# Kernel optimization log

Hardware: AMD Instinct MI355X
Metric: run time of the kernel (lower is better)

The kernel has to match this reference:

```python
import jax, jax.numpy as jnp
import numpy as np

DIM = 32          # d_model == channel dim of the volume
D_STATE = 16
D_CONV = 4
EXPAND = 2
D_INNER = EXPAND * DIM        # 64
DT_RANK = max(1, (DIM + 15) // 16)  # ceil(d_model/16) = 2
LN_EPS = 1e-5


def setup_inputs() -> dict:
    key = jax.random.key(0)
    ks = jax.random.split(key, 12)
    B, Dd, Hh, Ww = 1, 32, 32, 32
    sc = 0.02
    x = jax.random.normal(ks[0], (B, DIM, Dd, Hh, Ww), jnp.float32)
    ln_w = jnp.ones((DIM,), jnp.float32)
    ln_b = jnp.zeros((DIM,), jnp.float32)
    in_proj_w = jax.random.normal(ks[1], (2 * D_INNER, DIM), jnp.float32) * sc
    conv_w = jax.random.normal(ks[2], (D_INNER, 1, D_CONV), jnp.float32) * sc
    conv_b = jnp.zeros((D_INNER,), jnp.float32)
    x_proj_w = jax.random.normal(ks[3], (DT_RANK + 2 * D_STATE, D_INNER), jnp.float32) * sc
    dt_proj_w = jax.random.normal(ks[4], (D_INNER, DT_RANK), jnp.float32) * sc
    dt_proj_b = jax.random.uniform(ks[5], (D_INNER,), jnp.float32, -4.0, -2.0)  # small softplus(dt) at init
    # Mamba S4D-real init: A = -[1..d_state], stored as A_log
    A_log = jnp.log(jnp.broadcast_to(jnp.arange(1, D_STATE + 1, dtype=jnp.float32), (D_INNER, D_STATE)))
    D_param = jnp.ones((D_INNER,), jnp.float32)
    out_proj_w = jax.random.normal(ks[6], (DIM, D_INNER), jnp.float32) * sc
    return {
        "x": x, "ln_w": ln_w, "ln_b": ln_b, "in_proj_w": in_proj_w,
        "conv_w": conv_w, "conv_b": conv_b, "x_proj_w": x_proj_w,
        "dt_proj_w": dt_proj_w, "dt_proj_b": dt_proj_b, "A_log": A_log,
        "D_param": D_param, "out_proj_w": out_proj_w,
    }


def _mamba_layer(x, ln_w, ln_b, in_proj_w, conv_w, conv_b, x_proj_w,
                 dt_proj_w, dt_proj_b, A_log, D_param, out_proj_w):
    B, C, Dd, Hh, Ww = x.shape
    L = Dd * Hh * Ww
    # z-scan flatten: (B, C, D, H, W) -> (B, L, C)
    xf = x.reshape(B, C, L).transpose(0, 2, 1)
    # LayerNorm over channel dim
    mu = jnp.mean(xf, axis=-1, keepdims=True)
    var = jnp.mean(jnp.square(xf - mu), axis=-1, keepdims=True)
    xn = (xf - mu) * jax.lax.rsqrt(var + LN_EPS) * ln_w + ln_b
    # in_proj -> x, z branches
    xz = xn @ in_proj_w.T                      # (B, L, 2*d_inner)
    x_in, z = jnp.split(xz, 2, axis=-1)
    # depthwise causal conv1d over sequence
    xt = x_in.transpose(0, 2, 1)               # (B, d_inner, L)
    xc = jax.lax.conv_general_dilated(
        xt, conv_w, window_strides=(1,), padding=[(D_CONV - 1, 0)],
        feature_group_count=D_INNER)
    xc = jax.nn.silu(xc + conv_b[None, :, None]).transpose(0, 2, 1)  # (B, L, d_inner)
    # input-dependent dt, B, C
    x_dbl = xc @ x_proj_w.T                    # (B, L, dt_rank + 2*d_state)
    dt, Bm, Cm = jnp.split(x_dbl, [DT_RANK, DT_RANK + D_STATE], axis=-1)
    delta = jax.nn.softplus(dt @ dt_proj_w.T + dt_proj_b)            # (B, L, d_inner)
    A = -jnp.exp(A_log)                        # (d_inner, d_state)
    # discretize: h_t = exp(delta*A) h_{t-1} + delta*B_t*x_t
    dA = jnp.exp(delta[..., None] * A)                               # (B, L, d_inner, d_state)
    dBx = delta[..., None] * Bm[:, :, None, :] * xc[..., None]       # (B, L, d_inner, d_state)
    def comb(e1, e2):
        a1, b1 = e1
        a2, b2 = e2
        return (a1 * a2, a2 * b1 + b2)
    _, h = jax.lax.associative_scan(comb, (dA, dBx), axis=1)         # parallel linear recurrence
    y = jnp.einsum('blds,bls->bld', h, Cm) + xc * D_param            # (B, L, d_inner)
    y = y * jax.nn.silu(z)
    out = y @ out_proj_w.T                     # (B, L, C)
    # unpermute z-scan
    return out.transpose(0, 2, 1).reshape(B, C, Dd, Hh, Ww)


def reference(x, ln_w, ln_b, in_proj_w, conv_w, conv_b, x_proj_w,
              dt_proj_w, dt_proj_b, A_log, D_param, out_proj_w):
    return _mamba_layer(x, ln_w, ln_b, in_proj_w, conv_w, conv_b, x_proj_w,
                        dt_proj_w, dt_proj_b, A_log, D_param, out_proj_w)
```

## Files before the change

kernel.cpp:

```cpp
#include <hip/hip_runtime.h>
#include <hip/hip_bf16.h>

constexpr int L   = 32768;
constexpr int CD  = 32;
constexpr int DI  = 64;
constexpr int DS  = 16;
constexpr int LC  = 64;
constexpr int NCH = L / LC;
constexpr int NPAIR = DI * DS;

constexpr size_t FL        = (size_t)DI * L;
constexpr size_t OFF_SZ    = 0;
constexpr size_t OFF_XC    = FL;
constexpr size_t OFF_DELTA = 2 * FL;
constexpr size_t OFF_BM    = 3 * FL;
constexpr size_t OFF_CM    = OFF_BM + (size_t)DS * L;
constexpr size_t OFF_APROD = OFF_CM + (size_t)DS * L;
constexpr size_t OFF_CARRY = OFF_APROD;
constexpr size_t OFF_BACC  = OFF_APROD + (size_t)NCH * NPAIR;

__device__ __forceinline__ float bf2f(__hip_bfloat16 v) { return __bfloat162float(v); }
__device__ __forceinline__ void f4arr(const float4 v, float* a) { a[0]=v.x; a[1]=v.y; a[2]=v.z; a[3]=v.w; }

__device__ __forceinline__ bool detect_bf16(const void* ln_w) {
    return ((const unsigned short*)ln_w)[0] == 0x3F80;
}
__device__ __forceinline__ float ldin(const void* p, size_t i, bool bf16) {
    return bf16 ? bf2f(((const __hip_bfloat16*)p)[i]) : ((const float*)p)[i];
}

__device__ __forceinline__ float dot32_g(const void* w, int row, const float* xv, bool isb) {
    float acc = 0.f;
    if (isb) {
        const __hip_bfloat16* p = (const __hip_bfloat16*)w + (size_t)row * 32;
        #pragma unroll
        for (int c = 0; c < 32; ++c) acc += bf2f(p[c]) * xv[c];
    } else {
        const float4* p = (const float4*)((const float*)w + (size_t)row * 32);
        #pragma unroll
        for (int q = 0; q < 8; ++q) {
            const float4 w4 = p[q];
            acc += w4.x * xv[4*q] + w4.y * xv[4*q+1] + w4.z * xv[4*q+2] + w4.w * xv[4*q+3];
        }
    }
    return acc;
}

__global__ __launch_bounds__(256, 3) void k12_featurize_scan(
    const void* __restrict__ x,
    const void* __restrict__ ln_w,
    const void* __restrict__ ln_b,
    const void* __restrict__ in_proj_w,
    const void* __restrict__ conv_w,
    const void* __restrict__ conv_b,
    const void* __restrict__ x_proj_w,
    const void* __restrict__ dt_proj_w,
    const void* __restrict__ dt_proj_b,
    const void* __restrict__ A_log,
    float* __restrict__ ws)
{
    __shared__ __align__(16) char smem[53648];
    float (*xin_s)[68]  = (float(*)[68])(smem);
    float (*sxc)[68]    = (float(*)[68])(smem);
    char* AR = smem + 17408;
    float (*xn_s)[33]   = (float(*)[33])(AR);
    float (*w_in_s)[32] = (float(*)[32])(AR + 8848);
    float (*sdl)[68]    = (float(*)[68])(AR);
    float (*sbm)[68]    = (float(*)[68])(AR + 17408);
    char* FW = smem + 42640;
    float (*w_xp)[64]   = (float(*)[64])(FW);
    float (*w_cv)[4]    = (float(*)[4])(FW + 8704);
    float (*w_dt)[2]    = (float(*)[2])(FW + 9728);
    float* b_dt_s = (float*)(FW + 10240);
    float* b_cv_s = (float*)(FW + 10496);
    float* lnw_s  = (float*)(FW + 10752);
    float* lnb_s  = (float*)(FW + 10880);

    const int tid = threadIdx.x;
    const int l0  = blockIdx.x * LC;
    const bool isb = detect_bf16(ln_w);

    if (isb) {
        const __hip_bfloat16* ipw = (const __hip_bfloat16*)in_proj_w;
        const __hip_bfloat16* xpw = (const __hip_bfloat16*)x_proj_w;
        for (int i = tid; i < 128 * 32; i += 256) w_in_s[i >> 5][i & 31] = bf2f(ipw[i]);
        for (int i = tid; i < 34 * 64; i += 256)  w_xp[i >> 6][i & 63] = bf2f(xpw[i]);
    } else {
        const float* ipw = (const float*)in_proj_w;
        const float* xpw = (const float*)x_proj_w;
        for (int i = tid; i < 128 * 32; i += 256) w_in_s[i >> 5][i & 31] = ipw[i];
        for (int i = tid; i < 34 * 64; i += 256)  w_xp[i >> 6][i & 63] = xpw[i];
    }
    w_cv[tid >> 2][tid & 3] = ldin(conv_w, tid, isb);
    if (tid < 128) w_dt[tid >> 1][tid & 1] = ldin(dt_proj_w, tid, isb);
    if (tid < 64) { b_dt_s[tid] = ldin(dt_proj_b, tid, isb); b_cv_s[tid] = ldin(conv_b, tid, isb); }
    if (tid < 32) { lnw_s[tid] = ldin(ln_w, tid, isb); lnb_s[tid] = ldin(ln_b, tid, isb); }
    __syncthreads();

    if (tid < LC + 3) {
        const int l = l0 - 3 + tid;
        const bool valid = (l >= 0);
        const int lc = valid ? l : 0;
        float xv[CD];
        if (isb) {
            const __hip_bfloat16* xb = (const __hip_bfloat16*)x;
            #pragma unroll
            for (int c = 0; c < CD; ++c) xv[c] = bf2f(xb[(size_t)c * L + lc]);
        } else {
            const float* xf = (const float*)x;
            #pragma unroll
            for (int c = 0; c < CD; ++c) xv[c] = xf[(size_t)c * L + lc];
        }
        float mu = 0.f;
        #pragma unroll
        for (int c = 0; c < CD; ++c) mu += xv[c];
        mu *= (1.f / CD);
        float var = 0.f;
        #pragma unroll
        for (int c = 0; c < CD; ++c) { const float dc = xv[c] - mu; var += dc * dc; }
        const float rstd = rsqrtf(var * (1.f / CD) + 1e-5f);
        #pragma unroll
        for (int c = 0; c < CD; ++c)
            xn_s[tid][c] = valid ? ((xv[c] - mu) * rstd * lnw_s[c] + lnb_s[c]) : 0.f;
    }
    __syncthreads();

    {
        const int wv   = tid >> 6;
        const int lane = tid & 63;
        const int jb   = wv * 32;
        if (wv < 2) {
            float xv0[CD];
            #pragma unroll
            for (int c = 0; c < CD; ++c) xv0[c] = xn_s[lane][c];
            for (int j = 0; j < 32; ++j) {
                const float4* wr = (const float4*)w_in_s[jb + j];
                float a0 = 0.f;
                #pragma unroll
                for (int q = 0; q < 8; ++q) {
                    const float4 w4 = wr[q];
                    a0 += w4.x * xv0[4*q] + w4.y * xv0[4*q+1] + w4.z * xv0[4*q+2] + w4.w * xv0[4*q+3];
                }
                xin_s[jb + j][lane] = a0;
            }
        } else {
            const int l = l0 + lane;
            float xv[CD];
            #pragma unroll
            for (int c = 0; c < CD; ++c) xv[c] = xn_s[3 + lane][c];
            for (int j = 0; j < 32; ++j) {
                const float4* wr = (const float4*)w_in_s[jb + j];
                float acc = 0.f;
                #pragma unroll
                for (int q = 0; q < 8; ++q) {
                    const float4 w4 = wr[q];
                    acc += w4.x * xv[4*q] + w4.y * xv[4*q+1] + w4.z * xv[4*q+2] + w4.w * xv[4*q+3];
                }
                const float s = acc / (1.f + __expf(-acc));
                ws[OFF_SZ + (size_t)(jb - 64 + j) * L + l] = s;
            }
            {
                const int col0 = (wv == 2) ? 64 : 65;
                float xvh[CD];
                #pragma unroll
                for (int c = 0; c < CD; ++c) xvh[c] = xn_s[col0][c];
                xin_s[lane][col0] = dot32_g(in_proj_w, lane, xvh, isb);
                if (wv == 3) {
                    #pragma unroll
                    for (int c = 0; c < CD; ++c) xvh[c] = xn_s[66][c];
                    xin_s[lane][66] = dot32_g(in_proj_w, lane, xvh, isb);
                }
            }
        }
    }
    __syncthreads();

    {
        const int h  = tid & 3;
        const int pq = tid >> 2;
        const int l  = l0 + pq;
        const int dbase = h * 16;
        float xcv[16];
        #pragma unroll
        for (int i = 0; i < 16; ++i) {
            const int d = dbase + i;
            float acc = b_cv_s[d];
            #pragma unroll
            for (int k = 0; k < 4; ++k) acc += w_cv[d][k] * xin_s[d][pq + k];
            const float v = acc / (1.f + __expf(-acc));
            xcv[i] = v;
            ws[OFF_XC + (size_t)d * L + l] = v;
        }
        float dt0 = 0.f, dt1 = 0.f;
        for (int r = 0; r < 34; ++r) {
            float acc = 0.f;
            #pragma unroll
            for (int i = 0; i < 16; ++i) acc += w_xp[r][dbase + i] * xcv[i];
            acc += __shfl_xor(acc, 1);
            acc += __shfl_xor(acc, 2);
            if (r == 0) dt0 = acc;
            else if (r == 1) dt1 = acc;
            else {
                const int rr = r - 2;
                if (h == (rr >> 3)) {
                    const size_t off = (rr < 16) ? (OFF_BM + (size_t)rr * L)
                                                 : (OFF_CM + (size_t)(rr - 16) * L);
                    ws[off + l] = acc;
                    if (rr < 16) sbm[rr][pq] = acc;
                }
            }
        }
        #pragma unroll
        for (int i = 0; i < 16; ++i) {
            const int d = dbase + i;
            const float tv = dt0 * w_dt[d][0] + dt1 * w_dt[d][1] + b_dt_s[d];
            const float sp = fmaxf(tv, 0.f) + log1pf(__expf(-fabsf(tv)));
            ws[OFF_DELTA + (size_t)d * L + l] = sp;
            sdl[d][pq] = sp;
        }
        __syncthreads();
        #pragma unroll
        for (int i = 0; i < 16; ++i) sxc[dbase + i][pq] = xcv[i];
    }
    __syncthreads();

    {
        const int d = tid >> 2, sg = tid & 3;
        float Aj[4], ap[4] = {1.f, 1.f, 1.f, 1.f}, bb[4] = {0.f, 0.f, 0.f, 0.f};
        #pragma unroll
        for (int j = 0; j < 4; ++j) Aj[j] = -__expf(ldin(A_log, d * DS + sg + 4 * j, isb));

        for (int t = 0; t < LC; t += 4) {
            float ddv[4], xxv[4], bm[4][4];
            f4arr(*(const float4*)&sdl[d][t], ddv);
            f4arr(*(const float4*)&sxc[d][t], xxv);
            f4arr(*(const float4*)&sbm[sg][t],      bm[0]);
            f4arr(*(const float4*)&sbm[sg + 4][t],  bm[1]);
            f4arr(*(const float4*)&sbm[sg + 8][t],  bm[2]);
            f4arr(*(const float4*)&sbm[sg + 12][t], bm[3]);
            #pragma unroll
            for (int tt = 0; tt < 4; ++tt) {
                const float dxc = ddv[tt] * xxv[tt];
                #pragma unroll
                for (int j = 0; j < 4; ++j) {
                    const float e = __expf(ddv[tt] * Aj[j]);
                    ap[j] *= e;
                    bb[j] = e * bb[j] + dxc * bm[j][tt];
                }
            }
        }
        *(float4*)&ws[OFF_APROD + (size_t)blockIdx.x * NPAIR + tid * 4] = make_float4(ap[0], ap[1], ap[2], ap[3]);
        *(float4*)&ws[OFF_BACC  + (size_t)blockIdx.x * NPAIR + tid * 4] = make_float4(bb[0], bb[1], bb[2], bb[3]);
    }
}

__global__ __launch_bounds__(256) void k3_carry(float* __restrict__ ws)
{
    __shared__ float ctile[4][512];
    const int lane = threadIdx.x & 63;
    const int wv   = threadIdx.x >> 6;
    const int p    = blockIdx.x * 4 + wv;

    float a[8], b[8];
    #pragma unroll
    for (int i = 0; i < 8; ++i) {
        const size_t ch = (size_t)(lane * 8 + i);
        a[i] = ws[OFF_APROD + ch * NPAIR + p];
        b[i] = ws[OFF_BACC  + ch * NPAIR + p];
    }

    float Ag = a[0], Bg = b[0];
    #pragma unroll
    for (int i = 1; i < 8; ++i) { Bg = a[i] * Bg + b[i]; Ag = Ag * a[i]; }
    #pragma unroll
    for (int off = 1; off < 64; off <<= 1) {
        const float pa = __shfl_up(Ag, off);
        const float pb = __shfl_up(Bg, off);
        if (lane >= off) { Bg = Ag * pb + Bg; Ag = Ag * pa; }
    }
    float Pb = __shfl_up(Bg, 1);
    if (lane == 0) Pb = 0.f;
    #pragma unroll
    for (int i = 0; i < 8; ++i) { ctile[wv][lane * 8 + i] = Pb; Pb = a[i] * Pb + b[i]; }
    __syncthreads();
    #pragma unroll
    for (int r = 0; r < 2; ++r) {
        const int ch = threadIdx.x + 256 * r;
        *(float4*)&ws[OFF_CARRY + (size_t)ch * NPAIR + blockIdx.x * 4] =
            make_float4(ctile[0][ch], ctile[1][ch], ctile[2][ch], ctile[3][ch]);
    }
}

__global__ __launch_bounds__(256, 4) void k45_apply_out(
    const void* __restrict__ A_log,
    const void* __restrict__ D_param,
    const void* __restrict__ ln_w,
    const void* __restrict__ out_proj_w,
    float* __restrict__ ws,
    void* __restrict__ out)
{
    __shared__ __align__(16) char smem45[26112];
    float (*sy)[68]      = (float(*)[68])(smem45);
    float (*sbm)[68]     = (float(*)[68])(smem45 + 17408);
    float (*scm)[68]     = (float(*)[68])(smem45 + 21760);
    float (*w_out_s)[64] = (float(*)[64])(smem45 + 17408);

    const int tid = threadIdx.x;
    const int c   = blockIdx.x;
    const size_t t0 = (size_t)c * LC;
    const bool isb = detect_bf16(ln_w);

    {
        const int r = tid >> 4, t4 = (tid & 15) * 4;
        *(float4*)&sbm[r][t4] = *(const float4*)&ws[OFF_BM + (size_t)r * L + t0 + t4];
        *(float4*)&scm[r][t4] = *(const float4*)&ws[OFF_CM + (size_t)r * L + t0 + t4];
    }

    const int d = tid >> 2, sg = tid & 3;
    float Aj[4];
    #pragma unroll
    for (int j = 0; j < 4; ++j) Aj[j] = -__expf(ldin(A_log, d * DS + sg + 4 * j, isb));
    const float Dd = ldin(D_param, d, isb);
    float hh[4];
    {
        const float4 h4 = *(const float4*)&ws[OFF_CARRY + (size_t)c * NPAIR + tid * 4];
        hh[0] = h4.x; hh[1] = h4.y; hh[2] = h4.z; hh[3] = h4.w;
    }
    __syncthreads();

    const float* dlp = ws + OFF_DELTA + (size_t)d * L + t0;
    const float* xcp = ws + OFF_XC    + (size_t)d * L + t0;
    float4 dd4 = *(const float4*)dlp;
    float4 xx4 = *(const float4*)xcp;
    for (int t = 0; t < LC; t += 4) {
        const int tn = (t + 4) & 63;
        const float4 ddn = *(const float4*)(dlp + tn);
        const float4 xxn = *(const float4*)(xcp + tn);
        float ddv[4], xxv[4], bm[4][4], cm[4][4];
        f4arr(dd4, ddv);
        f4arr(xx4, xxv);
        f4arr(*(const float4*)&sbm[sg][t],      bm[0]);
        f4arr(*(const float4*)&sbm[sg + 4][t],  bm[1]);
        f4arr(*(const float4*)&sbm[sg + 8][t],  bm[2]);
        f4arr(*(const float4*)&sbm[sg + 12][t], bm[3]);
        f4arr(*(const float4*)&scm[sg][t],      cm[0]);
        f4arr(*(const float4*)&scm[sg + 4][t],  cm[1]);
        f4arr(*(const float4*)&scm[sg + 8][t],  cm[2]);
        f4arr(*(const float4*)&scm[sg + 12][t], cm[3]);
        #pragma unroll
        for (int tt = 0; tt < 4; ++tt) {
            const float dxc = ddv[tt] * xxv[tt];
            float ys = 0.f;
            #pragma unroll
            for (int j = 0; j < 4; ++j) {
                const float e = __expf(ddv[tt] * Aj[j]);
                hh[j] = e * hh[j] + dxc * bm[j][tt];
                ys += hh[j] * cm[j][tt];
            }
            ys += __shfl_xor(ys, 1);
            ys += __shfl_xor(ys, 2);
            if (sg == 0) sy[d][t + tt] = ys + xxv[tt] * Dd;
        }
        dd4 = ddn; xx4 = xxn;
    }
    __syncthreads();

    if (isb) {
        const __hip_bfloat16* opw = (const __hip_bfloat16*)out_proj_w;
        for (int i = tid; i < CD * DI; i += 256) w_out_s[i >> 6][i & 63] = bf2f(opw[i]);
    } else {
        const float* opw = (const float*)out_proj_w;
        for (int i = tid; i < CD * DI; i += 256) w_out_s[i >> 6][i & 63] = opw[i];
    }

    #pragma unroll
    for (int k = 0; k < 4; ++k) {
        const int idx = tid + k * 256;
        const int r = idx >> 4, t4 = (idx & 15) * 4;
        float4 yv = *(float4*)&sy[r][t4];
        const float4 zv = *(const float4*)&ws[OFF_SZ + (size_t)r * L + t0 + t4];
        yv.x *= zv.x; yv.y *= zv.y; yv.z *= zv.z; yv.w *= zv.w;
        *(float4*)&sy[r][t4] = yv;
    }
    __syncthreads();

    {
        const int wv   = tid >> 6;
        const int lane = tid & 63;
        float acc[8] = {0.f, 0.f, 0.f, 0.f, 0.f, 0.f, 0.f, 0.f};
        for (int dd = 0; dd < DI; ++dd) {
            const float yv = sy[dd][lane];
            #pragma unroll
            for (int j = 0; j < 8; ++j)
                acc[j] += yv * w_out_s[wv * 8 + j][dd];
        }
        const size_t l = t0 + lane;
        #pragma unroll
        for (int j = 0; j < 8; ++j) {
            const int cc = wv * 8 + j;
            if (isb) ((__hip_bfloat16*)out)[(size_t)cc * L + l] = __float2bfloat16(acc[j]);
            else     ((float*)out)[(size_t)cc * L + l] = acc[j];
        }
    }
}

extern "C" void kernel_launch(void* const* d_in, const int* in_sizes, int n_in,
                              void* d_out, int out_size, void* d_ws, size_t ws_size,
                              hipStream_t stream)
{
    (void)in_sizes; (void)n_in; (void)out_size; (void)ws_size;
    const void* x        = d_in[0];
    const void* ln_w     = d_in[1];
    const void* ln_b     = d_in[2];
    const void* in_pw    = d_in[3];
    const void* conv_w   = d_in[4];
    const void* conv_b   = d_in[5];
    const void* x_pw     = d_in[6];
    const void* dt_pw    = d_in[7];
    const void* dt_pb    = d_in[8];
    const void* A_log    = d_in[9];
    const void* D_param  = d_in[10];
    const void* out_pw   = d_in[11];
    float* ws = (float*)d_ws;

    k12_featurize_scan<<<NCH, 256, 0, stream>>>(x, ln_w, ln_b, in_pw, conv_w, conv_b,
                                                x_pw, dt_pw, dt_pb, A_log, ws);
    k3_carry<<<NPAIR / 4, 256, 0, stream>>>(ws);
    k45_apply_out<<<NCH, 256, 0, stream>>>(A_log, D_param, ln_w, out_pw, ws, d_out);
}
```

Before: 154.7 us.

## Recompute gate branch in apply kernel and halve chunk length

The silu(z) gate is no longer computed in the featurize kernel and stored to workspace. The apply/out kernel instead reloads x, redoes the LayerNorm and the z half of in_proj, and applies silu locally. This removes a 64xL float write plus a later reread. The chunk length drops from 64 to 32, which doubles the chunk count and the carry-kernel work per pair, shrinks shared memory, and raises the occupancy hint. The cost is redundant LayerNorm arithmetic, extra reads of x, and a larger carry array.

```diff
diff --git a/kernel.cpp b/kernel.cpp
--- a/kernel.cpp
+++ b/kernel.cpp
@@ -5,15 +5,14 @@
 constexpr int CD  = 32;
 constexpr int DI  = 64;
 constexpr int DS  = 16;
-constexpr int LC  = 64;
+constexpr int LC  = 32;
 constexpr int NCH = L / LC;
 constexpr int NPAIR = DI * DS;
 
 constexpr size_t FL        = (size_t)DI * L;
-constexpr size_t OFF_SZ    = 0;
-constexpr size_t OFF_XC    = FL;
-constexpr size_t OFF_DELTA = 2 * FL;
-constexpr size_t OFF_BM    = 3 * FL;
+constexpr size_t OFF_XC    = 0;
+constexpr size_t OFF_DELTA = FL;
+constexpr size_t OFF_BM    = 2 * FL;
 constexpr size_t OFF_CM    = OFF_BM + (size_t)DS * L;
 constexpr size_t OFF_APROD = OFF_CM + (size_t)DS * L;
 constexpr size_t OFF_CARRY = OFF_APROD;
@@ -46,7 +45,7 @@
     return acc;
 }
 
-__global__ __launch_bounds__(256, 3) void k12_featurize_scan(
+__global__ __launch_bounds__(256, 4) void k12_featurize_scan(
     const void* __restrict__ x,
     const void* __restrict__ ln_w,
     const void* __restrict__ ln_b,
@@ -59,15 +58,15 @@
     const void* __restrict__ A_log,
     float* __restrict__ ws)
 {
-    __shared__ __align__(16) char smem[53648];
-    float (*xin_s)[68]  = (float(*)[68])(smem);
-    float (*sxc)[68]    = (float(*)[68])(smem);
-    char* AR = smem + 17408;
+    __shared__ __align__(16) char smem[33040];
+    float (*xin_s)[36]  = (float(*)[36])(smem);
+    float (*sxc)[36]    = (float(*)[36])(smem);
+    char* AR = smem + 9216;
     float (*xn_s)[33]   = (float(*)[33])(AR);
-    float (*w_in_s)[32] = (float(*)[32])(AR + 8848);
-    float (*sdl)[68]    = (float(*)[68])(AR);
-    float (*sbm)[68]    = (float(*)[68])(AR + 17408);
-    char* FW = smem + 42640;
+    float (*w_in_s)[32] = (float(*)[32])(AR + 4624);
+    float (*sdl)[36]    = (float(*)[36])(AR);
+    float (*sbm)[36]    = (float(*)[36])(AR + 9216);
+    char* FW = smem + 22032;
     float (*w_xp)[64]   = (float(*)[64])(FW);
     float (*w_cv)[4]    = (float(*)[4])(FW + 8704);
     float (*w_dt)[2]    = (float(*)[2])(FW + 9728);
@@ -83,13 +82,14 @@
     if (isb) {
         const __hip_bfloat16* ipw = (const __hip_bfloat16*)in_proj_w;
         const __hip_bfloat16* xpw = (const __hip_bfloat16*)x_proj_w;
-        for (int i = tid; i < 128 * 32; i += 256) w_in_s[i >> 5][i & 31] = bf2f(ipw[i]);
-        for (int i = tid; i < 34 * 64; i += 256)  w_xp[i >> 6][i & 63] = bf2f(xpw[i]);
+        for (int i = tid; i < 64 * 32; i += 256) ((float*)w_in_s)[i] = bf2f(ipw[i]);
+        for (int i = tid; i < 34 * 64; i += 256) ((float*)w_xp)[i] = bf2f(xpw[i]);
     } else {
-        const float* ipw = (const float*)in_proj_w;
-        const float* xpw = (const float*)x_proj_w;
-        for (int i = tid; i < 128 * 32; i += 256) w_in_s[i >> 5][i & 31] = ipw[i];
-        for (int i = tid; i < 34 * 64; i += 256)  w_xp[i >> 6][i & 63] = xpw[i];
+        const float4* ipw = (const float4*)in_proj_w;
+        const float4* xpw = (const float4*)x_proj_w;
+        #pragma unroll
+        for (int k = 0; k < 2; ++k) ((float4*)w_in_s)[tid + 256 * k] = ipw[tid + 256 * k];
+        for (int i = tid; i < 544; i += 256) ((float4*)w_xp)[i] = xpw[i];
     }
     w_cv[tid >> 2][tid & 3] = ldin(conv_w, tid, isb);
     if (tid < 128) w_dt[tid >> 1][tid & 1] = ldin(dt_proj_w, tid, isb);
@@ -126,63 +126,42 @@
     __syncthreads();
 
     {
-        const int wv   = tid >> 6;
-        const int lane = tid & 63;
-        const int jb   = wv * 32;
-        if (wv < 2) {
-            float xv0[CD];
-            #pragma unroll
-            for (int c = 0; c < CD; ++c) xv0[c] = xn_s[lane][c];
-            for (int j = 0; j < 32; ++j) {
-                const float4* wr = (const float4*)w_in_s[jb + j];
-                float a0 = 0.f;
-                #pragma unroll
-                for (int q = 0; q < 8; ++q) {
-                    const float4 w4 = wr[q];
-                    a0 += w4.x * xv0[4*q] + w4.y * xv0[4*q+1] + w4.z * xv0[4*q+2] + w4.w * xv0[4*q+3];
-                }
-                xin_s[jb + j][lane] = a0;
+        const int colq = tid & 31;
+        const int rgrp = tid >> 5;
+        float xv[CD];
+        #pragma unroll
+        for (int c = 0; c < CD; ++c) xv[c] = xn_s[colq][c];
+        #pragma unroll
+        for (int j = 0; j < 8; ++j) {
+            const int row = rgrp * 8 + j;
+            const float4* wr = (const float4*)w_in_s[row];
+            float a0 = 0.f;
+            #pragma unroll
+            for (int q = 0; q < 8; ++q) {
+                const float4 w4 = wr[q];
+                a0 += w4.x * xv[4*q] + w4.y * xv[4*q+1] + w4.z * xv[4*q+2] + w4.w * xv[4*q+3];
             }
-        } else {
-            const int l = l0 + lane;
-            float xv[CD];
-            #pragma unroll
-            for (int c = 0; c < CD; ++c) xv[c] = xn_s[3 + lane][c];
-            for (int j = 0; j < 32; ++j) {
-                const float4* wr = (const float4*)w_in_s[jb + j];
-                float acc = 0.f;
-                #pragma unroll
-                for (int q = 0; q < 8; ++q) {
-                    const float4 w4 = wr[q];
-                    acc += w4.x * xv[4*q] + w4.y * xv[4*q+1] + w4.z * xv[4*q+2] + w4.w * xv[4*q+3];
-                }
-                const float s = acc / (1.f + __expf(-acc));
-                ws[OFF_SZ + (size_t)(jb - 64 + j) * L + l] = s;
-            }
-            {
-                const int col0 = (wv == 2) ? 64 : 65;
-                float xvh[CD];
-                #pragma unroll
-                for (int c = 0; c < CD; ++c) xvh[c] = xn_s[col0][c];
-                xin_s[lane][col0] = dot32_g(in_proj_w, lane, xvh, isb);
-                if (wv == 3) {
-                    #pragma unroll
-                    for (int c = 0; c < CD; ++c) xvh[c] = xn_s[66][c];
-                    xin_s[lane][66] = dot32_g(in_proj_w, lane, xvh, isb);
-                }
-            }
-        }
-    }
-    __syncthreads();
-
-    {
-        const int h  = tid & 3;
-        const int pq = tid >> 2;
+            xin_s[row][colq] = a0;
+        }
+        if (tid < 192) {
+            const int row = tid & 63;
+            const int cH  = 32 + (tid >> 6);
+            float xvh[CD];
+            #pragma unroll
+            for (int c = 0; c < CD; ++c) xvh[c] = xn_s[cH][c];
+            xin_s[row][cH] = dot32_g(in_proj_w, row, xvh, isb);
+        }
+    }
+    __syncthreads();
+
+    {
+        const int h  = tid & 7;
+        const int pq = tid >> 3;
         const int l  = l0 + pq;
-        const int dbase = h * 16;
-        float xcv[16];
-        #pragma unroll
-        for (int i = 0; i < 16; ++i) {
+        const int dbase = h * 8;
+        float xcv[8];
+        #pragma unroll
+        for (int i = 0; i < 8; ++i) {
             const int d = dbase + i;
             float acc = b_cv_s[d];
             #pragma unroll
@@ -195,14 +174,15 @@
         for (int r = 0; r < 34; ++r) {
             float acc = 0.f;
             #pragma unroll
-            for (int i = 0; i < 16; ++i) acc += w_xp[r][dbase + i] * xcv[i];
+            for (int i = 0; i < 8; ++i) acc += w_xp[r][dbase + i] * xcv[i];
             acc += __shfl_xor(acc, 1);
             acc += __shfl_xor(acc, 2);
+            acc += __shfl_xor(acc, 4);
             if (r == 0) dt0 = acc;
             else if (r == 1) dt1 = acc;
             else {
                 const int rr = r - 2;
-                if (h == (rr >> 3)) {
+                if (h == (rr >> 2)) {
                     const size_t off = (rr < 16) ? (OFF_BM + (size_t)rr * L)
                                                  : (OFF_CM + (size_t)(rr - 16) * L);
                     ws[off + l] = acc;
@@ -211,7 +191,7 @@
             }
         }
         #pragma unroll
-        for (int i = 0; i < 16; ++i) {
+        for (int i = 0; i < 8; ++i) {
             const int d = dbase + i;
             const float tv = dt0 * w_dt[d][0] + dt1 * w_dt[d][1] + b_dt_s[d];
             const float sp = fmaxf(tv, 0.f) + log1pf(__expf(-fabsf(tv)));
@@ -220,7 +200,7 @@
         }
         __syncthreads();
         #pragma unroll
-        for (int i = 0; i < 16; ++i) sxc[dbase + i][pq] = xcv[i];
+        for (int i = 0; i < 8; ++i) sxc[dbase + i][pq] = xcv[i];
     }
     __syncthreads();
 
@@ -256,22 +236,22 @@
 
 __global__ __launch_bounds__(256) void k3_carry(float* __restrict__ ws)
 {
-    __shared__ float ctile[4][512];
+    __shared__ float ctile[4][NCH];
     const int lane = threadIdx.x & 63;
     const int wv   = threadIdx.x >> 6;
     const int p    = blockIdx.x * 4 + wv;
 
-    float a[8], b[8];
-    #pragma unroll
-    for (int i = 0; i < 8; ++i) {
-        const size_t ch = (size_t)(lane * 8 + i);
+    float a[16], b[16];
+    #pragma unroll
+    for (int i = 0; i < 16; ++i) {
+        const size_t ch = (size_t)(lane * 16 + i);
         a[i] = ws[OFF_APROD + ch * NPAIR + p];
         b[i] = ws[OFF_BACC  + ch * NPAIR + p];
     }
 
     float Ag = a[0], Bg = b[0];
     #pragma unroll
-    for (int i = 1; i < 8; ++i) { Bg = a[i] * Bg + b[i]; Ag = Ag * a[i]; }
+    for (int i = 1; i < 16; ++i) { Bg = a[i] * Bg + b[i]; Ag = Ag * a[i]; }
     #pragma unroll
     for (int off = 1; off < 64; off <<= 1) {
         const float pa = __shfl_up(Ag, off);
@@ -281,10 +261,10 @@
     float Pb = __shfl_up(Bg, 1);
     if (lane == 0) Pb = 0.f;
     #pragma unroll
-    for (int i = 0; i < 8; ++i) { ctile[wv][lane * 8 + i] = Pb; Pb = a[i] * Pb + b[i]; }
-    __syncthreads();
-    #pragma unroll
-    for (int r = 0; r < 2; ++r) {
+    for (int i = 0; i < 16; ++i) { ctile[wv][lane * 16 + i] = Pb; Pb = a[i] * Pb + b[i]; }
+    __syncthreads();
+    #pragma unroll
+    for (int r = 0; r < 4; ++r) {
         const int ch = threadIdx.x + 256 * r;
         *(float4*)&ws[OFF_CARRY + (size_t)ch * NPAIR + blockIdx.x * 4] =
             make_float4(ctile[0][ch], ctile[1][ch], ctile[2][ch], ctile[3][ch]);
@@ -292,18 +272,24 @@
 }
 
 __global__ __launch_bounds__(256, 4) void k45_apply_out(
+    const void* __restrict__ x,
+    const void* __restrict__ ln_w,
+    const void* __restrict__ ln_b,
+    const void* __restrict__ in_proj_w,
     const void* __restrict__ A_log,
     const void* __restrict__ D_param,
-    const void* __restrict__ ln_w,
     const void* __restrict__ out_proj_w,
     float* __restrict__ ws,
     void* __restrict__ out)
 {
-    __shared__ __align__(16) char smem45[26112];
-    float (*sy)[68]      = (float(*)[68])(smem45);
-    float (*sbm)[68]     = (float(*)[68])(smem45 + 17408);
-    float (*scm)[68]     = (float(*)[68])(smem45 + 21760);
-    float (*w_out_s)[64] = (float(*)[64])(smem45 + 17408);
+    __shared__ __align__(16) char smem45[26880];
+    float (*sx)[36]      = (float(*)[36])(smem45);
+    float (*sy)[36]      = (float(*)[36])(smem45 + 4608);
+    float (*sbm)[36]     = (float(*)[36])(smem45 + 13824);
+    float (*scm)[36]     = (float(*)[36])(smem45 + 16128);
+    float (*w_out_s)[64] = (float(*)[64])(smem45 + 18432);
+    float* lnw_s = (float*)(smem45 + 26624);
+    float* lnb_s = (float*)(smem45 + 26752);
 
     const int tid = threadIdx.x;
     const int c   = blockIdx.x;
@@ -311,10 +297,31 @@
     const bool isb = detect_bf16(ln_w);
 
     {
-        const int r = tid >> 4, t4 = (tid & 15) * 4;
-        *(float4*)&sbm[r][t4] = *(const float4*)&ws[OFF_BM + (size_t)r * L + t0 + t4];
-        *(float4*)&scm[r][t4] = *(const float4*)&ws[OFF_CM + (size_t)r * L + t0 + t4];
-    }
+        const int r = tid >> 3, t4 = (tid & 7) * 4;
+        if (isb) {
+            const __hip_bfloat16* xb = (const __hip_bfloat16*)x;
+            #pragma unroll
+            for (int k = 0; k < 4; ++k) sx[r][t4 + k] = bf2f(xb[(size_t)r * L + t0 + t4 + k]);
+        } else {
+            *(float4*)&sx[r][t4] = *(const float4*)&((const float*)x)[(size_t)r * L + t0 + t4];
+        }
+    }
+    {
+        const int q = tid & 127;
+        const int r = q >> 3, t4 = (q & 7) * 4;
+        const size_t src = ((tid < 128) ? OFF_BM : OFF_CM) + (size_t)r * L + t0 + t4;
+        float* dst = (tid < 128) ? &sbm[r][t4] : &scm[r][t4];
+        *(float4*)dst = *(const float4*)&ws[src];
+    }
+    if (isb) {
+        const __hip_bfloat16* opw = (const __hip_bfloat16*)out_proj_w;
+        for (int i = tid; i < CD * DI; i += 256) ((float*)w_out_s)[i] = bf2f(opw[i]);
+    } else {
+        const float4* opw = (const float4*)out_proj_w;
+        #pragma unroll
+        for (int k = 0; k < 2; ++k) ((float4*)w_out_s)[tid + 256 * k] = opw[tid + 256 * k];
+    }
+    if (tid < 32) { lnw_s[tid] = ldin(ln_w, tid, isb); lnb_s[tid] = ldin(ln_b, tid, isb); }
 
     const int d = tid >> 2, sg = tid & 3;
     float Aj[4];
@@ -326,14 +333,39 @@
         const float4 h4 = *(const float4*)&ws[OFF_CARRY + (size_t)c * NPAIR + tid * 4];
         hh[0] = h4.x; hh[1] = h4.y; hh[2] = h4.z; hh[3] = h4.w;
     }
-    __syncthreads();
-
     const float* dlp = ws + OFF_DELTA + (size_t)d * L + t0;
     const float* xcp = ws + OFF_XC    + (size_t)d * L + t0;
     float4 dd4 = *(const float4*)dlp;
     float4 xx4 = *(const float4*)xcp;
+    __syncthreads();
+
+    float szv[8];
+    {
+        const int pos  = tid & 31;
+        const int rgrp = tid >> 5;
+        float xnv[CD];
+        #pragma unroll
+        for (int ch = 0; ch < CD; ++ch) xnv[ch] = sx[ch][pos];
+        float mu = 0.f;
+        #pragma unroll
+        for (int ch = 0; ch < CD; ++ch) mu += xnv[ch];
+        mu *= (1.f / CD);
+        float var = 0.f;
+        #pragma unroll
+        for (int ch = 0; ch < CD; ++ch) { const float dc = xnv[ch] - mu; var += dc * dc; }
+        const float rstd = rsqrtf(var * (1.f / CD) + 1e-5f);
+        #pragma unroll
+        for (int ch = 0; ch < CD; ++ch) xnv[ch] = (xnv[ch] - mu) * rstd * lnw_s[ch] + lnb_s[ch];
+        #pragma unroll
+        for (int j = 0; j < 8; ++j) {
+            const int row = 64 + rgrp * 8 + j;
+            const float acc = dot32_g(in_proj_w, row, xnv, isb);
+            szv[j] = acc / (1.f + __expf(-acc));
+        }
+    }
+
     for (int t = 0; t < LC; t += 4) {
-        const int tn = (t + 4) & 63;
+        const int tn = (t + 4) & (LC - 1);
         const float4 ddn = *(const float4*)(dlp + tn);
         const float4 xxn = *(const float4*)(xcp + tn);
         float ddv[4], xxv[4], bm[4][4], cm[4][4];
@@ -365,39 +397,30 @@
     }
     __syncthreads();
 
-    if (isb) {
-        const __hip_bfloat16* opw = (const __hip_bfloat16*)out_proj_w;
-        for (int i = tid; i < CD * DI; i += 256) w_out_s[i >> 6][i & 63] = bf2f(opw[i]);
-    } else {
-        const float* opw = (const float*)out_proj_w;
-        for (int i = tid; i < CD * DI; i += 256) w_out_s[i >> 6][i & 63] = opw[i];
-    }
-
-    #pragma unroll
-    for (int k = 0; k < 4; ++k) {
-        const int idx = tid + k * 256;
-        const int r = idx >> 4, t4 = (idx & 15) * 4;
-        float4 yv = *(float4*)&sy[r][t4];
-        const float4 zv = *(const float4*)&ws[OFF_SZ + (size_t)r * L + t0 + t4];
-        yv.x *= zv.x; yv.y *= zv.y; yv.z *= zv.z; yv.w *= zv.w;
-        *(float4*)&sy[r][t4] = yv;
+    {
+        const int pos  = tid & 31;
+        const int rgrp = tid >> 5;
+        #pragma unroll
+        for (int j = 0; j < 8; ++j) sy[rgrp * 8 + j][pos] *= szv[j];
     }
     __syncthreads();
 
     {
         const int wv   = tid >> 6;
         const int lane = tid & 63;
-        float acc[8] = {0.f, 0.f, 0.f, 0.f, 0.f, 0.f, 0.f, 0.f};
+        const int pos  = lane & 31;
+        const int cg   = lane >> 5;
+        float acc[4] = {0.f, 0.f, 0.f, 0.f};
         for (int dd = 0; dd < DI; ++dd) {
-            const float yv = sy[dd][lane];
-            #pragma unroll
-            for (int j = 0; j < 8; ++j)
-                acc[j] += yv * w_out_s[wv * 8 + j][dd];
-        }
-        const size_t l = t0 + lane;
-        #pragma unroll
-        for (int j = 0; j < 8; ++j) {
-            const int cc = wv * 8 + j;
+            const float yv = sy[dd][pos];
+            #pragma unroll
+            for (int j = 0; j < 4; ++j)
+                acc[j] += yv * w_out_s[wv * 8 + cg * 4 + j][dd];
+        }
+        const size_t l = t0 + pos;
+        #pragma unroll
+        for (int j = 0; j < 4; ++j) {
+            const int cc = wv * 8 + cg * 4 + j;
             if (isb) ((__hip_bfloat16*)out)[(size_t)cc * L + l] = __float2bfloat16(acc[j]);
             else     ((float*)out)[(size_t)cc * L + l] = acc[j];
         }
@@ -426,5 +449,6 @@
     k12_featurize_scan<<<NCH, 256, 0, stream>>>(x, ln_w, ln_b, in_pw, conv_w, conv_b,
                                                 x_pw, dt_pw, dt_pb, A_log, ws);
     k3_carry<<<NPAIR / 4, 256, 0, stream>>>(ws);
-    k45_apply_out<<<NCH, 256, 0, stream>>>(A_log, D_param, ln_w, out_pw, ws, d_out);
-}
+    k45_apply_out<<<NCH, 256, 0, stream>>>(x, ln_w, ln_b, in_pw, A_log, D_param,
+                                           out_pw, ws, d_out);
+}
```

Measured after the change: 232.9 us. 50.5% more time.
